# Kernel optimization log

Hardware: AMD Instinct MI355X
Metric: run time of the kernel (lower is better)

The kernel has to match this reference:

```python
import jax, jax.numpy as jnp
import numpy as np

B, N, D, H = 8, 1024, 768, 12
HD = D // H
SCALE = HD ** -0.5

def setup_inputs() -> dict:
    key = jax.random.key(0)
    k1, k2, k3, k4 = jax.random.split(key, 4)
    x = jax.random.normal(k1, (B, N, D), dtype=jnp.float32)
    weight = jax.random.uniform(k2, (B, N), dtype=jnp.float32)
    W_qkv = jax.random.normal(k3, (D, 3 * D), dtype=jnp.float32) * (D ** -0.5)
    W_msa = jax.random.normal(k4, (D, D), dtype=jnp.float32) * (D ** -0.5)
    b_msa = jnp.zeros((D,), dtype=jnp.float32)
    return {"x": x, "weight": weight, "W_qkv": W_qkv, "W_msa": W_msa, "b_msa": b_msa}

def reference(x, weight, W_qkv, W_msa, b_msa):
    # QKV projection (no bias), then elementwise per-token gate
    qkv = jnp.einsum('bnd,de->bne', x, W_qkv)          # [B,N,3D]
    qkv = weight[:, :, None] * qkv
    qkv = qkv.reshape(B, N, 3, H, HD).transpose(2, 0, 3, 1, 4)  # [3,B,H,N,hd]
    q, k, v = qkv[0], qkv[1], qkv[2]
    A = jnp.einsum('bhnd,bhmd->bhnm', q, k) * SCALE    # [B,H,N,N]
    A = jax.nn.softmax(A, axis=-1)
    out = jnp.einsum('bhnm,bhmd->bhnd', A, v)          # [B,H,N,hd]
    out = out.transpose(0, 2, 1, 3).reshape(B, N, D)
    return jnp.einsum('bnd,de->bne', out, W_msa) + b_msa
```

## Files before the change

### kernel.cpp

```cpp
#include <hip/hip_runtime.h>
#include <hip/hip_bf16.h>


typedef __attribute__((ext_vector_type(8))) short bf8;
typedef __attribute__((ext_vector_type(4))) float f4;

#define QSCALE 0.1803368801111204f
#define MFMA16 __builtin_amdgcn_mfma_f32_16x16x32_bf16

static __device__ __forceinline__ short bf16_of(float f) {
    union { float f; unsigned u; } a; a.f = f;
    unsigned r = a.u + 0x7FFFu + ((a.u >> 16) & 1u);
    return (short)(r >> 16);
}

static __device__ __forceinline__ unsigned bfpk(float lo, float hi) {
    float2 t; t.x = lo; t.y = hi;
    __hip_bfloat162 b = __float22bfloat162_rn(t);
    union { __hip_bfloat162 b; unsigned u; } c; c.b = b;
    return c.u;
}

static __device__ __forceinline__ void async16(const short* g, short* l) {
    __builtin_amdgcn_global_load_lds(
        (const __attribute__((address_space(1))) void*)g,
        (__attribute__((address_space(3))) void*)l, 16, 0, 0);
}

static __device__ __forceinline__ void transpose64(
        const float* __restrict__ w, short* __restrict__ wt,
        int K, int E, int k0, int e0, int tid, short (*t)[65]) {
#pragma unroll
    for (int p = 0; p < 16; ++p) {
        int idx = p * 256 + tid;
        int r = idx >> 6, c = idx & 63;
        t[r][c] = bf16_of(w[(k0 + r) * E + e0 + c]);
    }
    __syncthreads();
#pragma unroll
    for (int p = 0; p < 16; ++p) {
        int idx = p * 256 + tid;
        int r = idx >> 6, c = idx & 63;
        wt[(e0 + r) * K + k0 + c] = t[c][r];
    }
}

__global__ __launch_bounds__(256) void k_prep(
        const float* __restrict__ x, const float* __restrict__ gate,
        short* __restrict__ xb,
        const float* __restrict__ Wqkv, short* __restrict__ wtq,
        const float* __restrict__ Wmsa, short* __restrict__ wtm) {
    __shared__ short t[64][65];
    const int bid = blockIdx.x, tid = threadIdx.x;
    if (bid < 3072) {
        int i = bid * 256 + tid;
        const float g = gate[i / 96];
        const f4* sp = (const f4*)x;
        f4 a = sp[2 * i], b = sp[2 * i + 1];
        union { bf8 v; short h[8]; } o;
        o.h[0] = bf16_of(a[0] * g); o.h[1] = bf16_of(a[1] * g);
        o.h[2] = bf16_of(a[2] * g); o.h[3] = bf16_of(a[3] * g);
        o.h[4] = bf16_of(b[0] * g); o.h[5] = bf16_of(b[1] * g);
        o.h[6] = bf16_of(b[2] * g); o.h[7] = bf16_of(b[3] * g);
        ((bf8*)xb)[i] = o.v;
    } else if (bid < 3504) {
        int tt = bid - 3072;
        transpose64(Wqkv, wtq, 768, 2304, (tt / 36) * 64, (tt % 36) * 64, tid, t);
    } else {
        int tt = bid - 3504;
        transpose64(Wmsa, wtm, 768, 768, (tt / 12) * 64, (tt % 12) * 64, tid, t);
    }
}

static __device__ __forceinline__ void gemm128(const short* __restrict__ gA,
                                               const short* __restrict__ gB,
                                               short* smem,
                                               f4 acc[4][4]) {
    const int tid = threadIdx.x, lane = tid & 63;
    const int l16 = lane & 15, quad = lane >> 4, rx = l16 & 7;
    const int wm = (tid >> 6) & 1, wn = tid >> 7;

    auto stage = [&](short* S, int k0) {
#pragma unroll
        for (int c = 0; c < 4; ++c) {
            int p = c * 256 + tid;
            int row = p >> 3, slot = p & 7;
            int gc = slot ^ (row & 7);
            async16(gA + row * 768 + k0 + gc * 8, S + p * 8);
            async16(gB + row * 768 + k0 + gc * 8, S + 8192 + p * 8);
        }
    };

    stage(smem, 0);
    for (int it = 0; it < 12; ++it) {
        __builtin_amdgcn_s_waitcnt(0);
        __syncthreads();
        short* Sc = smem + (it & 1) * 16384;
        if (it + 1 < 12) stage(smem + ((it + 1) & 1) * 16384, (it + 1) * 64);
        const short* As = Sc;
        const short* Bs = Sc + 8192;
#pragma unroll
        for (int ks = 0; ks < 2; ++ks) {
            bf8 af[4], bfr[4];
#pragma unroll
            for (int mt = 0; mt < 4; ++mt)
                af[mt] = *(const bf8*)(As + (wm * 64 + mt * 16 + l16) * 64 +
                                       (((ks * 4 + quad) ^ rx) * 8));
#pragma unroll
            for (int nt = 0; nt < 4; ++nt)
                bfr[nt] = *(const bf8*)(Bs + (wn * 64 + nt * 16 + l16) * 64 +
                                        (((ks * 4 + quad) ^ rx) * 8));
#pragma unroll
            for (int mt = 0; mt < 4; ++mt)
#pragma unroll
                for (int nt = 0; nt < 4; ++nt)
                    acc[mt][nt] = MFMA16(af[mt], bfr[nt], acc[mt][nt], 0, 0, 0);
        }
    }
    __syncthreads();
}

__global__ __launch_bounds__(256, 2) void k_gemm_qkv(
        const short* __restrict__ xb, const short* __restrict__ wtq,
        short* __restrict__ qb, short* __restrict__ kb, short* __restrict__ vt) {
    __shared__ short lds[34816];
    const int tid = threadIdx.x, lane = tid & 63;
    const int l16 = lane & 15, quad = lane >> 4, rx = l16 & 7;
    const int wm = tid >> 6;

    const int wg = blockIdx.x;
    const int swz = (wg & 7) * 128 + (wg >> 3);
    const int mI = swz >> 4, nI = swz & 15;
    const int m0 = mI * 128, n0 = nI * 144;

    const short* gA = xb + m0 * 768;
    const short* gB = wtq + n0 * 768;

    auto stageA = [&](int buf, int k0) {
        short* base = lds + buf * 17408;
#pragma unroll
        for (int j = 0; j < 4; ++j) {
            int p = j * 256 + tid, row = p >> 3;
            int gc = (p & 7) ^ (row & 7);
            async16(gA + row * 768 + k0 + gc * 8, base + p * 8);
        }
    };
    auto stageB = [&](int buf, int k0) {
        short* base = lds + buf * 17408 + 8192;
#pragma unroll
        for (int j = 0; j < 4; ++j) {
            int p = j * 256 + tid, row = p >> 3;
            int gc = (p & 7) ^ (row & 7);
            async16(gB + row * 768 + k0 + gc * 8, base + p * 8);
        }
        if (tid < 128) {
            int p = 1024 + tid, row = p >> 3;
            int gc = (p & 7) ^ (row & 7);
            async16(gB + row * 768 + k0 + gc * 8, base + p * 8);
        }
    };

    auto rdA = [&](const short* base, int mf, int ks) {
        return *(const bf8*)(base + (wm * 32 + mf * 16 + l16) * 64 +
                             (((ks * 4 + quad) ^ rx) << 3));
    };
    auto rdB = [&](const short* base, int nf, int ks) {
        return *(const bf8*)(base + 8192 + (nf * 16 + l16) * 64 +
                             (((ks * 4 + quad) ^ rx) << 3));
    };

    f4 z = {0.f, 0.f, 0.f, 0.f};
    f4 acc[2][9];
#pragma unroll
    for (int mf = 0; mf < 2; ++mf)
#pragma unroll
        for (int nf = 0; nf < 9; ++nf) acc[mf][nf] = z;

    stageA(0, 0); stageB(0, 0);
    asm volatile("s_waitcnt vmcnt(0)" ::: "memory");
    __builtin_amdgcn_s_barrier();

#pragma unroll 2
    for (int t = 0; t < 12; ++t) {
        const short* cur = lds + (t & 1) * 17408;
        bf8 af[2][2];
        af[0][0] = rdA(cur, 0, 0); af[0][1] = rdA(cur, 0, 1);
        af[1][0] = rdA(cur, 1, 0); af[1][1] = rdA(cur, 1, 1);
        bf8 bfr[5][2];
#pragma unroll
        for (int nf = 0; nf < 5; ++nf) { bfr[nf][0] = rdB(cur, nf, 0); bfr[nf][1] = rdB(cur, nf, 1); }
        if (t < 11) stageA((t + 1) & 1, (t + 1) * 64);
        __builtin_amdgcn_s_setprio(1);
#pragma unroll
        for (int mf = 0; mf < 2; ++mf)
#pragma unroll
            for (int nf = 0; nf < 5; ++nf) {
                acc[mf][nf] = MFMA16(af[mf][0], bfr[nf][0], acc[mf][nf], 0, 0, 0);
                acc[mf][nf] = MFMA16(af[mf][1], bfr[nf][1], acc[mf][nf], 0, 0, 0);
            }
        __builtin_amdgcn_s_setprio(0);
        bf8 bfh[4][2];
#pragma unroll
        for (int nf = 0; nf < 4; ++nf) { bfh[nf][0] = rdB(cur, nf + 5, 0); bfh[nf][1] = rdB(cur, nf + 5, 1); }
        if (t < 11) stageB((t + 1) & 1, (t + 1) * 64);
        __builtin_amdgcn_s_setprio(1);
#pragma unroll
        for (int mf = 0; mf < 2; ++mf)
#pragma unroll
            for (int nf = 0; nf < 4; ++nf) {
                acc[mf][nf + 5] = MFMA16(af[mf][0], bfh[nf][0], acc[mf][nf + 5], 0, 0, 0);
                acc[mf][nf + 5] = MFMA16(af[mf][1], bfh[nf][1], acc[mf][nf + 5], 0, 0, 0);
            }
        __builtin_amdgcn_s_setprio(0);
        asm volatile("s_waitcnt vmcnt(0)" ::: "memory");
        __builtin_amdgcn_s_barrier();
    }

    const int bI = m0 >> 10, nn0 = m0 & 1023;
#pragma unroll
    for (int nf = 0; nf < 9; ++nf) {
        const int ct = n0 + nf * 16;
        if (ct < 1536) {
            const int which = (ct >= 768) ? 1 : 0;
            const int h = (ct - which * 768) >> 6;
            const int hd = (ct & 63) + l16;
            short* dst = (which ? kb : qb) + (bI * 12 + h) * 65536 + hd;
#pragma unroll
            for (int mf = 0; mf < 2; ++mf)
#pragma unroll
                for (int r = 0; r < 4; ++r) {
                    const int nn = nn0 + wm * 32 + mf * 16 + quad * 4 + r;
                    const float val = acc[mf][nf][r];
                    dst[nn * 64] = bf16_of(which ? val : val * QSCALE);
                }
        }
    }
    const int vlo = (n0 >= 1536) ? n0 : 1536;
    const int vcnt = n0 + 144 - vlo;
    const int npass = (vcnt > 0) ? vcnt / 48 : 0;
    for (int p = 0; p < npass; ++p) {
        __syncthreads();
        const int c0 = vlo + p * 48;
#pragma unroll
        for (int nf = 0; nf < 9; ++nf) {
            const int ct = n0 + nf * 16;
            if (ct >= c0 && ct < c0 + 48) {
                const int lcol = ct - c0 + l16;
#pragma unroll
                for (int mf = 0; mf < 2; ++mf)
#pragma unroll
                    for (int r = 0; r < 4; ++r) {
                        const int row = wm * 32 + mf * 16 + quad * 4 + r;
                        lds[lcol * 136 + row] = bf16_of(acc[mf][nf][r]);
                    }
            }
        }
        __syncthreads();
        const int vg0 = c0 - 1536;
#pragma unroll
        for (int u = 0; u < 3; ++u) {
            const int idx = u * 256 + tid;
            const int lc = idx >> 4, ck = idx & 15;
            const int vg = vg0 + lc;
            const int h = vg >> 6, hd = vg & 63;
            bf8 vv = *(const bf8*)(lds + lc * 136 + ck * 8);
            *(bf8*)(vt + ((bI * 12 + h) * 64 + hd) * 1024 + nn0 + ck * 8) = vv;
        }
    }
}

__global__ __launch_bounds__(256) void k_gemm_final(
        const short* __restrict__ attn, const short* __restrict__ wtm,
        const float* __restrict__ bias, float* __restrict__ out) {
    __shared__ short smem[32768];
    const int lane = threadIdx.x & 63;
    const int l16 = lane & 15, quad = lane >> 4;
    const int wm = (threadIdx.x >> 6) & 1, wn = threadIdx.x >> 7;
    const int m0 = blockIdx.y * 128, n0 = blockIdx.x * 128;
    f4 z = {0.f, 0.f, 0.f, 0.f};
    f4 acc[4][4] = {{z,z,z,z},{z,z,z,z},{z,z,z,z},{z,z,z,z}};
    gemm128(attn + m0 * 768, wtm + n0 * 768, smem, acc);
#pragma unroll
    for (int mt = 0; mt < 4; ++mt) {
#pragma unroll
        for (int r = 0; r < 4; ++r) {
            const int row = m0 + wm * 64 + mt * 16 + quad * 4 + r;
#pragma unroll
            for (int nt = 0; nt < 4; ++nt) {
                const int e = n0 + wn * 64 + nt * 16 + l16;
                out[row * 768 + e] = acc[mt][nt][r] + bias[e];
            }
        }
    }
}

__global__ __launch_bounds__(256, 3) void k_attn(const short* __restrict__ qb,
                                                 const short* __restrict__ kb,
                                                 const short* __restrict__ vt,
                                                 short* __restrict__ attn) {
    __shared__ short Ks[2][4096];
    __shared__ short Vs[2][4096];
    const int tid = threadIdx.x, wave = tid >> 6, lane = tid & 63;
    const int l16 = lane & 15, quad = lane >> 4;
    const int bh = blockIdx.x;
    const int b = bh / 12, h = bh - b * 12;
    const int m_base = blockIdx.y * 128 + wave * 32;
    const short* qh = qb + bh * 65536;
    const short* kh = kb + bh * 65536;
    const short* vh = vt + bh * 65536;

    const int rA = ((l16 >> 2) << 3) + (l16 & 3);
    const int fK = (((rA >> 3) & 1) << 2) + (rA & 3);
    const int sK = (quad ^ fK) * 8;
    const int oAlo = rA * 64 + sK;
    const int oAhi = rA * 64 + (sK ^ 32);
    const int oBlo = oAlo + 256, oBhi = oAhi + 256;
    const int fV = (((l16 >> 3) & 1) << 2) + (l16 & 3);
    const int oV = l16 * 64 + ((quad ^ fV) * 8);

    const short* qp0 = qh + (m_base + l16) * 64 + quad * 8;
    bf8 qf00 = *(const bf8*)(qp0);
    bf8 qf01 = *(const bf8*)(qp0 + 32);
    const short* qp1 = qp0 + 16 * 64;
    bf8 qf10 = *(const bf8*)(qp1);
    bf8 qf11 = *(const bf8*)(qp1 + 32);

    union { bf8 v; short h[8]; } onef;
#pragma unroll
    for (int i = 0; i < 8; ++i) onef.h[i] = (short)0x3F80;

    f4 z = {0.f, 0.f, 0.f, 0.f};
    f4 acc0[4] = {z, z, z, z};
    f4 acc1[4] = {z, z, z, z};
    f4 accl0 = z, accl1 = z;

    auto stage = [&](int buf, int j0) {
#pragma unroll
        for (int j = 0; j < 2; ++j) {
            int idx = j * 256 + tid;
            int row = idx >> 3;
            int fr = (((row >> 3) & 1) << 2) + (row & 3);
            int gc = (idx & 7) ^ fr;
            async16(kh + (j0 + row) * 64 + gc * 8, Ks[buf] + idx * 8);
            async16(vh + row * 1024 + j0 + gc * 8, Vs[buf] + idx * 8);
        }
    };

    stage(0, 0);
    int cur = 0;
    for (int it = 0; it < 16; ++it) {
        __builtin_amdgcn_s_waitcnt(0);
        __syncthreads();
        if (it + 1 < 16) stage(cur ^ 1, (it + 1) * 64);
        const short* Kc = Ks[cur];
        const short* Vc = Vs[cur];

#pragma unroll
        for (int jj = 0; jj < 64; jj += 32) {
            const short* kjj = Kc + jj * 64;
            bf8 kAlo = *(const bf8*)(kjj + oAlo);
            bf8 kAhi = *(const bf8*)(kjj + oAhi);
            bf8 kBlo = *(const bf8*)(kjj + oBlo);
            bf8 kBhi = *(const bf8*)(kjj + oBhi);
            bf8 vf0 = *(const bf8*)(Vc + 0 * 1024 + (oV ^ (jj ? 32 : 0)));
            bf8 vf1 = *(const bf8*)(Vc + 1 * 1024 + (oV ^ (jj ? 32 : 0)));
            bf8 vf2 = *(const bf8*)(Vc + 2 * 1024 + (oV ^ (jj ? 32 : 0)));
            bf8 vf3 = *(const bf8*)(Vc + 3 * 1024 + (oV ^ (jj ? 32 : 0)));

            {
                f4 sA = z, sB = z;
                sA = MFMA16(kAlo, qf00, sA, 0, 0, 0);
                sA = MFMA16(kAhi, qf01, sA, 0, 0, 0);
                sB = MFMA16(kBlo, qf00, sB, 0, 0, 0);
                sB = MFMA16(kBhi, qf01, sB, 0, 0, 0);
                float a0 = __builtin_amdgcn_exp2f(sA[0]);
                float a1 = __builtin_amdgcn_exp2f(sA[1]);
                float a2 = __builtin_amdgcn_exp2f(sA[2]);
                float a3 = __builtin_amdgcn_exp2f(sA[3]);
                float b0 = __builtin_amdgcn_exp2f(sB[0]);
                float b1 = __builtin_amdgcn_exp2f(sB[1]);
                float b2 = __builtin_amdgcn_exp2f(sB[2]);
                float b3 = __builtin_amdgcn_exp2f(sB[3]);
                union { bf8 v; unsigned u[4]; } p;
                p.u[0] = bfpk(a0, a1); p.u[1] = bfpk(a2, a3);
                p.u[2] = bfpk(b0, b1); p.u[3] = bfpk(b2, b3);
                accl0 = MFMA16(onef.v, p.v, accl0, 0, 0, 0);
                acc0[0] = MFMA16(vf0, p.v, acc0[0], 0, 0, 0);
                acc0[1] = MFMA16(vf1, p.v, acc0[1], 0, 0, 0);
                acc0[2] = MFMA16(vf2, p.v, acc0[2], 0, 0, 0);
                acc0[3] = MFMA16(vf3, p.v, acc0[3], 0, 0, 0);
            }
            {
                f4 sA = z, sB = z;
                sA = MFMA16(kAlo, qf10, sA, 0, 0, 0);
                sA = MFMA16(kAhi, qf11, sA, 0, 0, 0);
                sB = MFMA16(kBlo, qf10, sB, 0, 0, 0);
                sB = MFMA16(kBhi, qf11, sB, 0, 0, 0);
                float a0 = __builtin_amdgcn_exp2f(sA[0]);
                float a1 = __builtin_amdgcn_exp2f(sA[1]);
                float a2 = __builtin_amdgcn_exp2f(sA[2]);
                float a3 = __builtin_amdgcn_exp2f(sA[3]);
                float b0 = __builtin_amdgcn_exp2f(sB[0]);
                float b1 = __builtin_amdgcn_exp2f(sB[1]);
                float b2 = __builtin_amdgcn_exp2f(sB[2]);
                float b3 = __builtin_amdgcn_exp2f(sB[3]);
                union { bf8 v; unsigned u[4]; } p;
                p.u[0] = bfpk(a0, a1); p.u[1] = bfpk(a2, a3);
                p.u[2] = bfpk(b0, b1); p.u[3] = bfpk(b2, b3);
                accl1 = MFMA16(onef.v, p.v, accl1, 0, 0, 0);
                acc1[0] = MFMA16(vf0, p.v, acc1[0], 0, 0, 0);
                acc1[1] = MFMA16(vf1, p.v, acc1[1], 0, 0, 0);
                acc1[2] = MFMA16(vf2, p.v, acc1[2], 0, 0, 0);
                acc1[3] = MFMA16(vf3, p.v, acc1[3], 0, 0, 0);
            }
        }
        cur ^= 1;
    }

    const float inv0 = 1.f / accl0[0];
    const float inv1 = 1.f / accl1[0];
    const int row0 = (b << 10) + m_base + l16;
    short* op0 = attn + row0 * 768 + h * 64 + quad * 4;
    short* op1 = op0 + 16 * 768;
#pragma unroll
    for (int dt = 0; dt < 4; ++dt)
#pragma unroll
        for (int r = 0; r < 4; ++r) {
            op0[dt * 16 + r] = bf16_of(acc0[dt][r] * inv0);
            op1[dt * 16 + r] = bf16_of(acc1[dt][r] * inv1);
        }
}

extern "C" void kernel_launch(void* const* d_in, const int* in_sizes, int n_in,
                              void* d_out, int out_size, void* d_ws, size_t ws_size,
                              hipStream_t stream) {
    const float* x    = (const float*)d_in[0];
    const float* gate = (const float*)d_in[1];
    const float* Wqkv = (const float*)d_in[2];
    const float* Wmsa = (const float*)d_in[3];
    const float* bmsa = (const float*)d_in[4];
    float* out = (float*)d_out;

    char* ws = (char*)d_ws;
    short* xb  = (short*)(ws);
    short* wtq = (short*)(ws + 12582912);
    short* wtm = (short*)(ws + 16121856);
    short* qb  = (short*)(ws + 17301504);
    short* kb  = (short*)(ws + 29884416);
    short* vt  = (short*)(ws + 42467328);
    short* attn = xb;

    k_prep<<<3648, 256, 0, stream>>>(x, gate, xb, Wqkv, wtq, Wmsa, wtm);
    k_gemm_qkv<<<1024, 256, 0, stream>>>(xb, wtq, qb, kb, vt);
    k_attn<<<dim3(96, 8), 256, 0, stream>>>(qb, kb, vt, attn);
    k_gemm_final<<<dim3(6, 64), 256, 0, stream>>>(attn, wtm, bmsa, out);
}
```

Measured before the change: 178.3 us.

## Retile output projection GEMM to 128x96 with swizzled grid and split staging

Replaces the 128x128 output-projection GEMM with a 128x96 tile kernel. It launches 512 workgroups on a swizzled 1D grid, gives each wave 32 rows, and issues the A and B async loads between the two MFMA halves so they overlap compute. The aim is better CU fill (512 blocks instead of 384), higher occupancy via launch bounds 2, and better L2 locality. It also wraps MFMA bursts in s_setprio in both the GEMM and the attention kernel, which raises wave priority around matrix-core work.

```diff
diff --git a/kernel.cpp b/kernel.cpp
--- a/kernel.cpp
+++ b/kernel.cpp
@@ -72,54 +72,6 @@
     }
 }
 
-static __device__ __forceinline__ void gemm128(const short* __restrict__ gA,
-                                               const short* __restrict__ gB,
-                                               short* smem,
-                                               f4 acc[4][4]) {
-    const int tid = threadIdx.x, lane = tid & 63;
-    const int l16 = lane & 15, quad = lane >> 4, rx = l16 & 7;
-    const int wm = (tid >> 6) & 1, wn = tid >> 7;
-
-    auto stage = [&](short* S, int k0) {
-#pragma unroll
-        for (int c = 0; c < 4; ++c) {
-            int p = c * 256 + tid;
-            int row = p >> 3, slot = p & 7;
-            int gc = slot ^ (row & 7);
-            async16(gA + row * 768 + k0 + gc * 8, S + p * 8);
-            async16(gB + row * 768 + k0 + gc * 8, S + 8192 + p * 8);
-        }
-    };
-
-    stage(smem, 0);
-    for (int it = 0; it < 12; ++it) {
-        __builtin_amdgcn_s_waitcnt(0);
-        __syncthreads();
-        short* Sc = smem + (it & 1) * 16384;
-        if (it + 1 < 12) stage(smem + ((it + 1) & 1) * 16384, (it + 1) * 64);
-        const short* As = Sc;
-        const short* Bs = Sc + 8192;
-#pragma unroll
-        for (int ks = 0; ks < 2; ++ks) {
-            bf8 af[4], bfr[4];
-#pragma unroll
-            for (int mt = 0; mt < 4; ++mt)
-                af[mt] = *(const bf8*)(As + (wm * 64 + mt * 16 + l16) * 64 +
-                                       (((ks * 4 + quad) ^ rx) * 8));
-#pragma unroll
-            for (int nt = 0; nt < 4; ++nt)
-                bfr[nt] = *(const bf8*)(Bs + (wn * 64 + nt * 16 + l16) * 64 +
-                                        (((ks * 4 + quad) ^ rx) * 8));
-#pragma unroll
-            for (int mt = 0; mt < 4; ++mt)
-#pragma unroll
-                for (int nt = 0; nt < 4; ++nt)
-                    acc[mt][nt] = MFMA16(af[mt], bfr[nt], acc[mt][nt], 0, 0, 0);
-        }
-    }
-    __syncthreads();
-}
-
 __global__ __launch_bounds__(256, 2) void k_gemm_qkv(
         const short* __restrict__ xb, const short* __restrict__ wtq,
         short* __restrict__ qb, short* __restrict__ kb, short* __restrict__ vt) {
@@ -269,28 +221,107 @@
     }
 }
 
-__global__ __launch_bounds__(256) void k_gemm_final(
+__global__ __launch_bounds__(256, 2) void k_gemm_final(
         const short* __restrict__ attn, const short* __restrict__ wtm,
         const float* __restrict__ bias, float* __restrict__ out) {
-    __shared__ short smem[32768];
-    const int lane = threadIdx.x & 63;
-    const int l16 = lane & 15, quad = lane >> 4;
-    const int wm = (threadIdx.x >> 6) & 1, wn = threadIdx.x >> 7;
-    const int m0 = blockIdx.y * 128, n0 = blockIdx.x * 128;
+    __shared__ short lds[28672];
+    const int tid = threadIdx.x, lane = tid & 63;
+    const int l16 = lane & 15, quad = lane >> 4, rx = l16 & 7;
+    const int wm = tid >> 6;
+
+    const int wg = blockIdx.x;
+    const int swz = (wg & 7) * 64 + (wg >> 3);
+    const int mI = swz >> 3, nI = swz & 7;
+    const int m0 = mI * 128, n0 = nI * 96;
+
+    const short* gA = attn + m0 * 768;
+    const short* gB = wtm + n0 * 768;
+
+    auto stageA = [&](int buf, int k0) {
+        short* base = lds + buf * 14336;
+#pragma unroll
+        for (int j = 0; j < 4; ++j) {
+            int p = j * 256 + tid, row = p >> 3;
+            int gc = (p & 7) ^ (row & 7);
+            async16(gA + row * 768 + k0 + gc * 8, base + p * 8);
+        }
+    };
+    auto stageB = [&](int buf, int k0) {
+        short* base = lds + buf * 14336 + 8192;
+#pragma unroll
+        for (int j = 0; j < 3; ++j) {
+            int p = j * 256 + tid, row = p >> 3;
+            int gc = (p & 7) ^ (row & 7);
+            async16(gB + row * 768 + k0 + gc * 8, base + p * 8);
+        }
+    };
+    auto rdA = [&](const short* base, int mf, int ks) {
+        return *(const bf8*)(base + (wm * 32 + mf * 16 + l16) * 64 +
+                             (((ks * 4 + quad) ^ rx) << 3));
+    };
+    auto rdB = [&](const short* base, int nf, int ks) {
+        return *(const bf8*)(base + 8192 + (nf * 16 + l16) * 64 +
+                             (((ks * 4 + quad) ^ rx) << 3));
+    };
+
     f4 z = {0.f, 0.f, 0.f, 0.f};
-    f4 acc[4][4] = {{z,z,z,z},{z,z,z,z},{z,z,z,z},{z,z,z,z}};
-    gemm128(attn + m0 * 768, wtm + n0 * 768, smem, acc);
-#pragma unroll
-    for (int mt = 0; mt < 4; ++mt) {
-#pragma unroll
-        for (int r = 0; r < 4; ++r) {
-            const int row = m0 + wm * 64 + mt * 16 + quad * 4 + r;
-#pragma unroll
-            for (int nt = 0; nt < 4; ++nt) {
-                const int e = n0 + wn * 64 + nt * 16 + l16;
-                out[row * 768 + e] = acc[mt][nt][r] + bias[e];
-            }
-        }
+    f4 acc[2][6];
+#pragma unroll
+    for (int mf = 0; mf < 2; ++mf)
+#pragma unroll
+        for (int nf = 0; nf < 6; ++nf) acc[mf][nf] = z;
+
+    stageA(0, 0); stageB(0, 0);
+    asm volatile("s_waitcnt vmcnt(0)" ::: "memory");
+    __builtin_amdgcn_s_barrier();
+
+#pragma unroll 2
+    for (int t = 0; t < 12; ++t) {
+        const short* cur = lds + (t & 1) * 14336;
+        bf8 af[2][2];
+        af[0][0] = rdA(cur, 0, 0); af[0][1] = rdA(cur, 0, 1);
+        af[1][0] = rdA(cur, 1, 0); af[1][1] = rdA(cur, 1, 1);
+        bf8 bfr[3][2];
+#pragma unroll
+        for (int nf = 0; nf < 3; ++nf) { bfr[nf][0] = rdB(cur, nf, 0); bfr[nf][1] = rdB(cur, nf, 1); }
+        if (t < 11) stageA((t + 1) & 1, (t + 1) * 64);
+        __builtin_amdgcn_s_setprio(1);
+#pragma unroll
+        for (int mf = 0; mf < 2; ++mf)
+#pragma unroll
+            for (int nf = 0; nf < 3; ++nf) {
+                acc[mf][nf] = MFMA16(af[mf][0], bfr[nf][0], acc[mf][nf], 0, 0, 0);
+                acc[mf][nf] = MFMA16(af[mf][1], bfr[nf][1], acc[mf][nf], 0, 0, 0);
+            }
+        __builtin_amdgcn_s_setprio(0);
+        bf8 bfh[3][2];
+#pragma unroll
+        for (int nf = 0; nf < 3; ++nf) { bfh[nf][0] = rdB(cur, nf + 3, 0); bfh[nf][1] = rdB(cur, nf + 3, 1); }
+        if (t < 11) stageB((t + 1) & 1, (t + 1) * 64);
+        __builtin_amdgcn_s_setprio(1);
+#pragma unroll
+        for (int mf = 0; mf < 2; ++mf)
+#pragma unroll
+            for (int nf = 0; nf < 3; ++nf) {
+                acc[mf][nf + 3] = MFMA16(af[mf][0], bfh[nf][0], acc[mf][nf + 3], 0, 0, 0);
+                acc[mf][nf + 3] = MFMA16(af[mf][1], bfh[nf][1], acc[mf][nf + 3], 0, 0, 0);
+            }
+        __builtin_amdgcn_s_setprio(0);
+        asm volatile("s_waitcnt vmcnt(0)" ::: "memory");
+        __builtin_amdgcn_s_barrier();
+    }
+
+#pragma unroll
+    for (int nf = 0; nf < 6; ++nf) {
+        const int e = n0 + nf * 16 + l16;
+        const float bv = bias[e];
+#pragma unroll
+        for (int mf = 0; mf < 2; ++mf)
+#pragma unroll
+            for (int r = 0; r < 4; ++r) {
+                const int row = m0 + wm * 32 + mf * 16 + quad * 4 + r;
+                out[row * 768 + e] = acc[mf][nf][r] + bv;
+            }
     }
 }
 
@@ -369,10 +400,12 @@
 
             {
                 f4 sA = z, sB = z;
+                __builtin_amdgcn_s_setprio(1);
                 sA = MFMA16(kAlo, qf00, sA, 0, 0, 0);
                 sA = MFMA16(kAhi, qf01, sA, 0, 0, 0);
                 sB = MFMA16(kBlo, qf00, sB, 0, 0, 0);
                 sB = MFMA16(kBhi, qf01, sB, 0, 0, 0);
+                __builtin_amdgcn_s_setprio(0);
                 float a0 = __builtin_amdgcn_exp2f(sA[0]);
                 float a1 = __builtin_amdgcn_exp2f(sA[1]);
                 float a2 = __builtin_amdgcn_exp2f(sA[2]);
@@ -384,18 +417,22 @@
                 union { bf8 v; unsigned u[4]; } p;
                 p.u[0] = bfpk(a0, a1); p.u[1] = bfpk(a2, a3);
                 p.u[2] = bfpk(b0, b1); p.u[3] = bfpk(b2, b3);
+                __builtin_amdgcn_s_setprio(1);
                 accl0 = MFMA16(onef.v, p.v, accl0, 0, 0, 0);
                 acc0[0] = MFMA16(vf0, p.v, acc0[0], 0, 0, 0);
                 acc0[1] = MFMA16(vf1, p.v, acc0[1], 0, 0, 0);
                 acc0[2] = MFMA16(vf2, p.v, acc0[2], 0, 0, 0);
                 acc0[3] = MFMA16(vf3, p.v, acc0[3], 0, 0, 0);
+                __builtin_amdgcn_s_setprio(0);
             }
             {
                 f4 sA = z, sB = z;
+                __builtin_amdgcn_s_setprio(1);
                 sA = MFMA16(kAlo, qf10, sA, 0, 0, 0);
                 sA = MFMA16(kAhi, qf11, sA, 0, 0, 0);
                 sB = MFMA16(kBlo, qf10, sB, 0, 0, 0);
                 sB = MFMA16(kBhi, qf11, sB, 0, 0, 0);
+                __builtin_amdgcn_s_setprio(0);
                 float a0 = __builtin_amdgcn_exp2f(sA[0]);
                 float a1 = __builtin_amdgcn_exp2f(sA[1]);
                 float a2 = __builtin_amdgcn_exp2f(sA[2]);
@@ -407,11 +444,13 @@
                 union { bf8 v; unsigned u[4]; } p;
                 p.u[0] = bfpk(a0, a1); p.u[1] = bfpk(a2, a3);
                 p.u[2] = bfpk(b0, b1); p.u[3] = bfpk(b2, b3);
+                __builtin_amdgcn_s_setprio(1);
                 accl1 = MFMA16(onef.v, p.v, accl1, 0, 0, 0);
                 acc1[0] = MFMA16(vf0, p.v, acc1[0], 0, 0, 0);
                 acc1[1] = MFMA16(vf1, p.v, acc1[1], 0, 0, 0);
                 acc1[2] = MFMA16(vf2, p.v, acc1[2], 0, 0, 0);
                 acc1[3] = MFMA16(vf3, p.v, acc1[3], 0, 0, 0);
+                __builtin_amdgcn_s_setprio(0);
             }
         }
         cur ^= 1;
@@ -453,5 +492,5 @@
     k_prep<<<3648, 256, 0, stream>>>(x, gate, xb, Wqkv, wtq, Wmsa, wtm);
     k_gemm_qkv<<<1024, 256, 0, stream>>>(xb, wtq, qb, kb, vt);
     k_attn<<<dim3(96, 8), 256, 0, stream>>>(qb, kb, vt, attn);
-    k_gemm_final<<<dim3(6, 64), 256, 0, stream>>>(attn, wtm, bmsa, out);
-}
+    k_gemm_final<<<512, 256, 0, stream>>>(attn, wtm, bmsa, out);
+}
```

Measured after the change: 179.0 us. Within noise of the previous version (+0.4%).
